# Performance work log

Hardware: AMD Instinct MI355X
Metric: run time of the kernel (lower is better)

The kernel has to match this reference:

```python
import jax, jax.numpy as jnp
import numpy as np

N, IN_FEATURES, OUT_FEATURES = 1048576, 32, 128


def setup_inputs() -> dict:
    key = jax.random.key(0)
    kx, kc = jax.random.split(key)
    x = jax.random.normal(kx, (N, IN_FEATURES), dtype=jnp.float32)
    # nn.init.normal_(centres, 0, 1); nn.init.constant_(log_sigmas, 0)
    centres = jax.random.normal(kc, (OUT_FEATURES, IN_FEATURES), dtype=jnp.float32)
    log_sigmas = jnp.zeros((OUT_FEATURES,), dtype=jnp.float32)
    return {"x": x, "centres": centres, "log_sigmas": log_sigmas}


def reference(x, centres, log_sigmas):
    x2 = jnp.sum(x * x, axis=-1, keepdims=True)            # (N, 1)
    c2 = jnp.sum(centres * centres, axis=-1)               # (out,)
    cross = jnp.einsum('ni,oi->no', x, centres)            # (N, out) GEMM
    sqdist = jnp.maximum(x2 - 2.0 * cross + c2, 0.0)       # clamp fp round-off
    # original: exp(-(sqrt(sqdist)/sigma)^2) == exp(-sqdist / sigma^2)
    inv_var = jnp.exp(-2.0 * log_sigmas)                   # (out,)
    return jnp.exp(-sqdist * inv_var)                      # (N, out)
```

## Files before the change

kernel.cpp:

```cpp
#include <hip/hip_runtime.h>

constexpr int IN_F   = 32;
constexpr int OUT_F  = 128;
constexpr int BLOCK  = 256;
constexpr int WAVES  = BLOCK / 64;
constexpr int RSTAGE = 16;

using f32x2 = __attribute__((ext_vector_type(2))) float;

__global__ __launch_bounds__(BLOCK, 4)
void rbf_kernel(const float* __restrict__ x,
                const float* __restrict__ centres,
                const float* __restrict__ log_sigmas,
                float* __restrict__ out,
                int rows_per_wave)
{
    __shared__ float4 xs[WAVES][2][RSTAGE][IN_F / 4];

    const int tid  = threadIdx.x;
    const int wv   = tid >> 6;
    const int lane = tid & 63;

    const int o0 = lane * 2;
    float c0[IN_F], c1[IN_F];
    float c2a = 0.f, c2b = 0.f;
    #pragma unroll
    for (int kc = 0; kc < IN_F / 4; ++kc) {
        const float4 a = *reinterpret_cast<const float4*>(centres + (size_t)(o0 + 0) * IN_F + kc * 4);
        const float4 b = *reinterpret_cast<const float4*>(centres + (size_t)(o0 + 1) * IN_F + kc * 4);
        c0[kc*4+0] = a.x; c0[kc*4+1] = a.y; c0[kc*4+2] = a.z; c0[kc*4+3] = a.w;
        c1[kc*4+0] = b.x; c1[kc*4+1] = b.y; c1[kc*4+2] = b.z; c1[kc*4+3] = b.w;
        c2a = fmaf(a.x,a.x,c2a); c2a = fmaf(a.y,a.y,c2a);
        c2a = fmaf(a.z,a.z,c2a); c2a = fmaf(a.w,a.w,c2a);
        c2b = fmaf(b.x,b.x,c2b); c2b = fmaf(b.y,b.y,c2b);
        c2b = fmaf(b.z,b.z,c2b); c2b = fmaf(b.w,b.w,c2b);
    }
    const float iv0 = __expf(-2.0f * log_sigmas[o0 + 0]);
    const float iv1 = __expf(-2.0f * log_sigmas[o0 + 1]);

    const size_t waveRow0 = ((size_t)blockIdx.x * WAVES + wv) * (size_t)rows_per_wave;
    const float* xbase = x + waveRow0 * IN_F;
    const int rs = lane >> 3;
    const int q  = lane & 7;

    float4 va = *reinterpret_cast<const float4*>(xbase + lane * 4);
    float4 vb = *reinterpret_cast<const float4*>(xbase + 8 * IN_F + lane * 4);

    int buf = 0;
    for (int it = 0; it < rows_per_wave; it += RSTAGE) {
        float sa = va.x * va.x;
        sa = fmaf(va.y, va.y, sa); sa = fmaf(va.z, va.z, sa); sa = fmaf(va.w, va.w, sa);
        sa += __shfl_xor(sa, 1); sa += __shfl_xor(sa, 2); sa += __shfl_xor(sa, 4);
        float sb = vb.x * vb.x;
        sb = fmaf(vb.y, vb.y, sb); sb = fmaf(vb.z, vb.z, sb); sb = fmaf(vb.w, vb.w, sb);
        sb += __shfl_xor(sb, 1); sb += __shfl_xor(sb, 2); sb += __shfl_xor(sb, 4);

        xs[wv][buf][rs][q]     = va;
        xs[wv][buf][8 + rs][q] = vb;

        if (it + RSTAGE < rows_per_wave) {
            const float* nxt = xbase + (size_t)(it + RSTAGE) * IN_F;
            va = *reinterpret_cast<const float4*>(nxt + lane * 4);
            vb = *reinterpret_cast<const float4*>(nxt + 8 * IN_F + lane * 4);
        }

        asm volatile("s_waitcnt lgkmcnt(0)" ::: "memory");

        #pragma unroll
        for (int rr = 0; rr < RSTAGE; ++rr) {
            float acc0 = 0.f, acc1 = 0.f;
            #pragma unroll
            for (int kc = 0; kc < IN_F / 4; ++kc) {
                const float4 xk = xs[wv][buf][rr][kc];
                acc0 = fmaf(xk.x, c0[kc*4+0], acc0);
                acc0 = fmaf(xk.y, c0[kc*4+1], acc0);
                acc0 = fmaf(xk.z, c0[kc*4+2], acc0);
                acc0 = fmaf(xk.w, c0[kc*4+3], acc0);
                acc1 = fmaf(xk.x, c1[kc*4+0], acc1);
                acc1 = fmaf(xk.y, c1[kc*4+1], acc1);
                acc1 = fmaf(xk.z, c1[kc*4+2], acc1);
                acc1 = fmaf(xk.w, c1[kc*4+3], acc1);
            }
            const float x2 = (rr < 8) ? __shfl(sa, rr * 8) : __shfl(sb, (rr - 8) * 8);
            const float t0 = fmaxf(fmaf(-2.0f, acc0, x2 + c2a), 0.0f);
            const float t1 = fmaxf(fmaf(-2.0f, acc1, x2 + c2b), 0.0f);
            f32x2 o;
            o.x = __expf(-t0 * iv0);
            o.y = __expf(-t1 * iv1);
            __builtin_nontemporal_store(o,
                reinterpret_cast<f32x2*>(out + (waveRow0 + it + rr) * OUT_F + o0));
        }
        buf ^= 1;
    }
}

extern "C" void kernel_launch(void* const* d_in, const int* in_sizes, int n_in,
                              void* d_out, int out_size, void* d_ws, size_t ws_size,
                              hipStream_t stream) {
    const float* x          = (const float*)d_in[0];
    const float* centres    = (const float*)d_in[1];
    const float* log_sigmas = (const float*)d_in[2];
    float* out = (float*)d_out;

    const int n = in_sizes[0] / IN_F;
    const int blocks = 2048;
    const int rows_per_block = n / blocks;
    const int rows_per_wave  = rows_per_block / WAVES;
    rbf_kernel<<<blocks, BLOCK, 0, stream>>>(x, centres, log_sigmas, out, rows_per_wave);
}
```

Before: 158.9 us.

## Split K across half-waves with packed FMA and permlane32 swap reduction

```diff
diff --git a/kernel.cpp b/kernel.cpp
--- a/kernel.cpp
+++ b/kernel.cpp
@@ -4,9 +4,13 @@
 constexpr int OUT_F  = 128;
 constexpr int BLOCK  = 256;
 constexpr int WAVES  = BLOCK / 64;
-constexpr int RSTAGE = 16;
+constexpr int RSTAGE = 8;
 
 using f32x2 = __attribute__((ext_vector_type(2))) float;
+
+__device__ __forceinline__ void swap32(float& a, float& b) {
+    asm volatile("v_permlane32_swap_b32 %0, %1" : "+v"(a), "+v"(b));
+}
 
 __global__ __launch_bounds__(BLOCK, 4)
 void rbf_kernel(const float* __restrict__ x,
@@ -20,77 +24,89 @@
     const int tid  = threadIdx.x;
     const int wv   = tid >> 6;
     const int lane = tid & 63;
+    const int j    = lane & 31;
+    const int h    = lane >> 5;
 
-    const int o0 = lane * 2;
-    float c0[IN_F], c1[IN_F];
-    float c2a = 0.f, c2b = 0.f;
+    f32x2 ch[4][8];
+    float q2[4];
     #pragma unroll
-    for (int kc = 0; kc < IN_F / 4; ++kc) {
-        const float4 a = *reinterpret_cast<const float4*>(centres + (size_t)(o0 + 0) * IN_F + kc * 4);
-        const float4 b = *reinterpret_cast<const float4*>(centres + (size_t)(o0 + 1) * IN_F + kc * 4);
-        c0[kc*4+0] = a.x; c0[kc*4+1] = a.y; c0[kc*4+2] = a.z; c0[kc*4+3] = a.w;
-        c1[kc*4+0] = b.x; c1[kc*4+1] = b.y; c1[kc*4+2] = b.z; c1[kc*4+3] = b.w;
-        c2a = fmaf(a.x,a.x,c2a); c2a = fmaf(a.y,a.y,c2a);
-        c2a = fmaf(a.z,a.z,c2a); c2a = fmaf(a.w,a.w,c2a);
-        c2b = fmaf(b.x,b.x,c2b); c2b = fmaf(b.y,b.y,c2b);
-        c2b = fmaf(b.z,b.z,c2b); c2b = fmaf(b.w,b.w,c2b);
+    for (int oo = 0; oo < 4; ++oo) {
+        const float* cp = centres + (size_t)(4 * j + oo) * IN_F + 16 * h;
+        float acc = 0.f;
+        #pragma unroll
+        for (int u = 0; u < 4; ++u) {
+            const float4 c4 = *reinterpret_cast<const float4*>(cp + 4 * u);
+            ch[oo][2*u+0] = (f32x2){c4.x, c4.y};
+            ch[oo][2*u+1] = (f32x2){c4.z, c4.w};
+            acc = fmaf(c4.x, c4.x, acc); acc = fmaf(c4.y, c4.y, acc);
+            acc = fmaf(c4.z, c4.z, acc); acc = fmaf(c4.w, c4.w, acc);
+        }
+        q2[oo] = acc;
     }
-    const float iv0 = __expf(-2.0f * log_sigmas[o0 + 0]);
-    const float iv1 = __expf(-2.0f * log_sigmas[o0 + 1]);
+    float a0 = q2[0], a1 = q2[1], a2 = q2[2], a3 = q2[3];
+    swap32(a2, a0); const float c2f0 = a2 + a0;
+    swap32(a3, a1); const float c2f1 = a3 + a1;
+    const int o_fin = 4 * j + 2 * (h ^ 1);
+    const float iv0 = __expf(-2.0f * log_sigmas[o_fin]);
+    const float iv1 = __expf(-2.0f * log_sigmas[o_fin + 1]);
 
     const size_t waveRow0 = ((size_t)blockIdx.x * WAVES + wv) * (size_t)rows_per_wave;
-    const float* xbase = x + waveRow0 * IN_F;
-    const int rs = lane >> 3;
-    const int q  = lane & 7;
+    const float* xb = x   + waveRow0 * IN_F;
+    float*       ob = out + waveRow0 * OUT_F + o_fin;
 
-    float4 va = *reinterpret_cast<const float4*>(xbase + lane * 4);
-    float4 vb = *reinterpret_cast<const float4*>(xbase + 8 * IN_F + lane * 4);
+    const int lr = lane >> 3;
+    const int lq = lane & 7;
 
-    int buf = 0;
+    float4 v0 = *reinterpret_cast<const float4*>(xb + lr * IN_F + lq * 4);
+    float4 vn = *reinterpret_cast<const float4*>(xb + (RSTAGE + lr) * IN_F + lq * 4);
+    xs[wv][0][lr][lq] = v0;
+
     for (int it = 0; it < rows_per_wave; it += RSTAGE) {
-        float sa = va.x * va.x;
-        sa = fmaf(va.y, va.y, sa); sa = fmaf(va.z, va.z, sa); sa = fmaf(va.w, va.w, sa);
-        sa += __shfl_xor(sa, 1); sa += __shfl_xor(sa, 2); sa += __shfl_xor(sa, 4);
-        float sb = vb.x * vb.x;
-        sb = fmaf(vb.y, vb.y, sb); sb = fmaf(vb.z, vb.z, sb); sb = fmaf(vb.w, vb.w, sb);
-        sb += __shfl_xor(sb, 1); sb += __shfl_xor(sb, 2); sb += __shfl_xor(sb, 4);
-
-        xs[wv][buf][rs][q]     = va;
-        xs[wv][buf][8 + rs][q] = vb;
-
+        const int buf = (it >> 3) & 1;
         if (it + RSTAGE < rows_per_wave) {
-            const float* nxt = xbase + (size_t)(it + RSTAGE) * IN_F;
-            va = *reinterpret_cast<const float4*>(nxt + lane * 4);
-            vb = *reinterpret_cast<const float4*>(nxt + 8 * IN_F + lane * 4);
+            xs[wv][buf ^ 1][lr][lq] = vn;
+            if (it + 2 * RSTAGE < rows_per_wave)
+                vn = *reinterpret_cast<const float4*>(
+                    xb + (size_t)(it + 2 * RSTAGE + lr) * IN_F + lq * 4);
         }
-
-        asm volatile("s_waitcnt lgkmcnt(0)" ::: "memory");
 
         #pragma unroll
         for (int rr = 0; rr < RSTAGE; ++rr) {
-            float acc0 = 0.f, acc1 = 0.f;
+            f32x2 p0 = {0.f,0.f}, p1 = {0.f,0.f}, p2 = {0.f,0.f}, p3 = {0.f,0.f};
+            f32x2 px = {0.f,0.f};
             #pragma unroll
-            for (int kc = 0; kc < IN_F / 4; ++kc) {
-                const float4 xk = xs[wv][buf][rr][kc];
-                acc0 = fmaf(xk.x, c0[kc*4+0], acc0);
-                acc0 = fmaf(xk.y, c0[kc*4+1], acc0);
-                acc0 = fmaf(xk.z, c0[kc*4+2], acc0);
-                acc0 = fmaf(xk.w, c0[kc*4+3], acc0);
-                acc1 = fmaf(xk.x, c1[kc*4+0], acc1);
-                acc1 = fmaf(xk.y, c1[kc*4+1], acc1);
-                acc1 = fmaf(xk.z, c1[kc*4+2], acc1);
-                acc1 = fmaf(xk.w, c1[kc*4+3], acc1);
+            for (int u = 0; u < 4; ++u) {
+                const float4 xq = xs[wv][buf][rr][h * 4 + u];
+                const f32x2 e0 = {xq.x, xq.y};
+                const f32x2 e1 = {xq.z, xq.w};
+                p0 = __builtin_elementwise_fma(e0, ch[0][2*u+0], p0);
+                p0 = __builtin_elementwise_fma(e1, ch[0][2*u+1], p0);
+                p1 = __builtin_elementwise_fma(e0, ch[1][2*u+0], p1);
+                p1 = __builtin_elementwise_fma(e1, ch[1][2*u+1], p1);
+                p2 = __builtin_elementwise_fma(e0, ch[2][2*u+0], p2);
+                p2 = __builtin_elementwise_fma(e1, ch[2][2*u+1], p2);
+                p3 = __builtin_elementwise_fma(e0, ch[3][2*u+0], p3);
+                p3 = __builtin_elementwise_fma(e1, ch[3][2*u+1], p3);
+                px = __builtin_elementwise_fma(e0, e0, px);
+                px = __builtin_elementwise_fma(e1, e1, px);
             }
-            const float x2 = (rr < 8) ? __shfl(sa, rr * 8) : __shfl(sb, (rr - 8) * 8);
-            const float t0 = fmaxf(fmaf(-2.0f, acc0, x2 + c2a), 0.0f);
-            const float t1 = fmaxf(fmaf(-2.0f, acc1, x2 + c2b), 0.0f);
+            float s0 = p0.x + p0.y, s1 = p1.x + p1.y;
+            float s2 = p2.x + p2.y, s3 = p3.x + p3.y;
+            float sxa = px.x + px.y, sxb = sxa;
+            swap32(s2, s0);
+            swap32(s3, s1);
+            swap32(sxa, sxb);
+            const float x2 = sxa + sxb;
+            const float d0 = s2 + s0;
+            const float d1 = s3 + s1;
+            const float t0 = fmaxf(fmaf(-2.0f, d0, x2 + c2f0), 0.0f);
+            const float t1 = fmaxf(fmaf(-2.0f, d1, x2 + c2f1), 0.0f);
             f32x2 o;
             o.x = __expf(-t0 * iv0);
             o.y = __expf(-t1 * iv1);
             __builtin_nontemporal_store(o,
-                reinterpret_cast<f32x2*>(out + (waveRow0 + it + rr) * OUT_F + o0));
+                reinterpret_cast<f32x2*>(ob + (size_t)(it + rr) * OUT_F));
         }
-        buf ^= 1;
     }
 }
 
@@ -103,8 +119,7 @@
     float* out = (float*)d_out;
 
     const int n = in_sizes[0] / IN_F;
-    const int blocks = 2048;
-    const int rows_per_block = n / blocks;
-    const int rows_per_wave  = rows_per_block / WAVES;
+    const int blocks = 4096;
+    const int rows_per_wave = n / (blocks * WAVES);
     rbf_kernel<<<blocks, BLOCK, 0, stream>>>(x, centres, log_sigmas, out, rows_per_wave);
 }
```

Measured after the change: 176.1 us. 1.11x slower.
